# Kernel optimization log

Hardware: AMD Instinct MI355X
Metric: run time of the kernel (lower is better)

## Reference

```python
import jax, jax.numpy as jnp
import numpy as np

N, C, H, W = 4, 256, 32, 32
NH = 2                      # att_nhead
HD = C // NH                # 128 per-head dim
MAX_DIS = 7
WS = 2 * MAX_DIS + 1        # 15 window side
WW = WS * WS                # 225 window positions
T = (C / NH) ** 0.5


def _gather_idx(h, w):
    # idx[wpos, m]: flat index into zero-padded (h+14, w+14) grid of the
    # neighbor at window offset wpos for query pixel m (== F.unfold semantics)
    pw = w + 2 * MAX_DIS
    dy, dx = np.meshgrid(np.arange(WS), np.arange(WS), indexing='ij')
    ys, xs = np.meshgrid(np.arange(h), np.arange(w), indexing='ij')
    idx = (dy.reshape(-1, 1) + ys.reshape(1, -1)) * pw + (dx.reshape(-1, 1) + xs.reshape(1, -1))
    return jnp.asarray(idx, dtype=jnp.int32)  # [WW, h*w]


def setup_inputs() -> dict:
    key = jax.random.key(0)
    ks = jax.random.split(key, 14)
    s = 0.02
    return {
        'q': jax.random.normal(ks[0], (N, C, H, W), jnp.float32),
        'k': jax.random.normal(ks[1], (N, C, H, W), jnp.float32),
        'v': jax.random.normal(ks[2], (N, C, H, W), jnp.float32),
        'Wq': jax.random.normal(ks[3], (C, C), jnp.float32) * s,
        'bq': jnp.zeros((C,), jnp.float32),
        'Wk': jax.random.normal(ks[4], (C, C), jnp.float32) * s,
        'bk': jnp.zeros((C,), jnp.float32),
        'Wv': jax.random.normal(ks[5], (C, C), jnp.float32) * s,
        'bv': jnp.zeros((C,), jnp.float32),
        'Wrel': jax.random.normal(ks[6], (NH, WW, HD), jnp.float32) * s,   # grouped 1x1 conv
        'brel': jnp.zeros((NH * WW,), jnp.float32),
        'V_bias': jax.random.normal(ks[7], (NH, HD, WW), jnp.float32) * s,
        'Wfc': jax.random.normal(ks[8], (C, C), jnp.float32) * s,
        'bfc': jnp.zeros((C,), jnp.float32),
    }


def _conv1x1(x, Wt, b):
    return jnp.einsum('nchw,dc->ndhw', x, Wt) + b[None, :, None, None]


def reference(q, k, v, Wq, bq, Wk, bk, Wv, bv, Wrel, brel, V_bias, Wfc, bfc):
    n, c, h, w = q.shape
    hw = h * w
    idx = _gather_idx(h, w)                                   # [WW, hw]
    pad = ((0, 0), (0, 0), (0, 0), (MAX_DIS, MAX_DIS), (MAX_DIS, MAX_DIS))

    q = _conv1x1(q, Wq, bq)
    k = _conv1x1(k, Wk, bk)
    v = _conv1x1(v, Wv, bv)

    # grouped 1x1 conv: relative position logits, [n, NH, WW, hw]
    rel = jnp.einsum('ngcxy,gwc->ngwxy', q.reshape(n, NH, HD, h, w), Wrel)
    rel = rel + brel.reshape(NH, WW)[None, :, :, None, None]
    rel = rel.reshape(n, NH, WW, hw)

    qs = (q / T).reshape(n, NH, HD, hw)

    # unfold K via zero-pad + gather: [n, NH, HD, WW, hw]
    k_pad = jnp.pad(k.reshape(n, NH, HD, h, w), pad).reshape(n, NH, HD, -1)
    k_un = k_pad[..., idx]
    qk = jnp.einsum('ngcm,ngcwm->ngwm', qs, k_un) + rel

    # boundary mask: neighbor inside the original image
    valid = jnp.pad(jnp.ones((h, w), jnp.float32), MAX_DIS).reshape(-1)[idx] > 0
    qk = jnp.where(valid[None, None], qk, jnp.float32(-1e8))
    attn = jax.nn.softmax(qk, axis=2)                         # over window positions

    agg_bias = jnp.einsum('ngwm,gcw->mngc', attn, V_bias).reshape(hw, n, c)

    # local2global scatter + dense einsum == gather of zero-padded V
    v_pad = jnp.pad(v.reshape(n, NH, HD, h, w), pad).reshape(n, NH, HD, -1)
    v_un = v_pad[..., idx]                                    # [n, NH, HD, WW, hw]
    agg_value = jnp.einsum('ngwm,ngcwm->mngc', attn, v_un).reshape(hw, n, c)

    out = (agg_value + agg_bias) @ Wfc.T + bfc                # [hw, n, c]
    return out
```

## Files before the change

kernel.cpp:

```cpp
#include <hip/hip_runtime.h>
#include <math.h>


typedef __attribute__((ext_vector_type(8))) short short8;
typedef __attribute__((ext_vector_type(4))) short short4v;
typedef __attribute__((ext_vector_type(4))) float floatx4;

__device__ __forceinline__ short f2bf(float f) {
    unsigned u = __float_as_uint(f);
    unsigned r = (u + 0x7fffu + ((u >> 16) & 1u)) >> 16;
    return (short)r;
}
__device__ __forceinline__ float bf2f(short s) {
    return __uint_as_float(((unsigned)(unsigned short)s) << 16);
}

__global__ __launch_bounds__(256)
void conv_kernel(const float* __restrict__ q, const float* __restrict__ k,
                 const float* __restrict__ v,
                 const float* __restrict__ Wq, const float* __restrict__ Wk,
                 const float* __restrict__ Wv, const float* __restrict__ Wfc,
                 const float* __restrict__ Wrel,
                 short* __restrict__ Xhi, short* __restrict__ Xlo,
                 short* __restrict__ Whi, short* __restrict__ Wlo,
                 short* __restrict__ Wrh, short* __restrict__ Wrl)
{
    const int tid = threadIdx.x;
    const int z = blockIdx.z;
    const int lane = tid & 63;
    const int n16 = lane & 15, quad = lane >> 4;

    if (z < 12) {
        __shared__ float st[64 * 33];
        const int sel = z >> 2, batch = z & 3;
        const float* X = (sel == 0 ? q : sel == 1 ? k : v) + ((long)batch << 18);
        const int mb = blockIdx.x, kc = blockIdx.y;
#pragma unroll
        for (int it = 0; it < 8; ++it) {
            int e = tid + it * 256;
            int cc = e >> 6, mm = e & 63;
            st[mm * 33 + cc] = X[((long)(kc * 32 + cc) << 10) + mb * 64 + mm];
        }
        __syncthreads();
        const int mtl = tid >> 6;
        const int m = mtl * 16 + n16;
        short h[8], l[8];
#pragma unroll
        for (int j = 0; j < 8; ++j) {
            float f = st[m * 33 + quad * 8 + j];
            short hb = f2bf(f);
            h[j] = hb;
            l[j] = f2bf(f - bf2f(hb));
        }
        int mt16 = mb * 4 + mtl;
        long off = (long)z * 262144 + (((long)(mt16 * 8 + kc) * 64) + lane) * 8;
        *(short8*)(Xhi + off) = *(short8*)&h[0];
        *(short8*)(Xlo + off) = *(short8*)&l[0];
    } else if (z < 16) {
        if (tid >= 64) return;
        const int w = z - 12;
        const float* W = (w == 0 ? Wq : w == 1 ? Wk : w == 2 ? Wv : Wfc);
        const int dt = blockIdx.x, kc = blockIdx.y;
        const int d = dt * 16 + n16, cb = kc * 32 + quad * 8;
        float4 w0 = *(const float4*)&W[d * 256 + cb];
        float4 w1 = *(const float4*)&W[d * 256 + cb + 4];
        float f[8] = {w0.x, w0.y, w0.z, w0.w, w1.x, w1.y, w1.z, w1.w};
        short h[8], l[8];
#pragma unroll
        for (int j = 0; j < 8; ++j) {
            short hb = f2bf(f[j]);
            h[j] = hb;
            l[j] = f2bf(f[j] - bf2f(hb));
        }
        long off = (long)w * 65536 + (((long)(dt * 8 + kc) * 64) + lane) * 8;
        *(short8*)(Whi + off) = *(short8*)&h[0];
        *(short8*)(Wlo + off) = *(short8*)&l[0];
    } else {
        if (tid >= 64) return;
        const int g = z - 16;
        const int wt = blockIdx.x, kc = blockIdx.y;
        if (wt >= 15 || kc >= 4) return;
        const int w = wt * 16 + n16;
        const int cb = kc * 32 + quad * 8;
        float f[8] = {0.f, 0.f, 0.f, 0.f, 0.f, 0.f, 0.f, 0.f};
        if (w < 225) {
            float4 w0 = *(const float4*)&Wrel[(long)(g * 225 + w) * 128 + cb];
            float4 w1 = *(const float4*)&Wrel[(long)(g * 225 + w) * 128 + cb + 4];
            f[0] = w0.x; f[1] = w0.y; f[2] = w0.z; f[3] = w0.w;
            f[4] = w1.x; f[5] = w1.y; f[6] = w1.z; f[7] = w1.w;
        }
        short h[8], l[8];
#pragma unroll
        for (int j = 0; j < 8; ++j) {
            short hb = f2bf(f[j]);
            h[j] = hb;
            l[j] = f2bf(f[j] - bf2f(hb));
        }
        long off = (long)g * 30720 + (((long)(wt * 4 + kc) * 64) + lane) * 8;
        *(short8*)(Wrh + off) = *(short8*)&h[0];
        *(short8*)(Wrl + off) = *(short8*)&l[0];
    }
}

__global__ __launch_bounds__(256)
void mfma_proj(const short* __restrict__ Xhi, const short* __restrict__ Xlo,
               const short* __restrict__ Whi, const short* __restrict__ Wlo,
               const float* __restrict__ bq, const float* __restrict__ bk,
               const float* __restrict__ bv,
               short* __restrict__ qhi, short* __restrict__ qlo,
               short* __restrict__ khi, short* __restrict__ klo,
               float* __restrict__ vpad)
{
    __shared__ float tile[16 * 65];
    const int tid = threadIdx.x;
    const int wave = tid >> 6, lane = tid & 63;
    const int n16 = lane & 15, quad = lane >> 4;
    const int mt16 = blockIdx.x, db = blockIdx.y, z = blockIdx.z;
    const int sel = z >> 2, batch = z & 3;
    const int dt = db * 4 + wave;

    const short* Ah = Whi + (long)sel * 65536 + ((long)(dt * 8) * 64 + lane) * 8;
    const short* Al = Wlo + (long)sel * 65536 + ((long)(dt * 8) * 64 + lane) * 8;
    const short* Bh = Xhi + (long)z * 262144;
    const short* Bl = Xlo + (long)z * 262144;

    const float* bias = (sel == 0 ? bq : sel == 1 ? bk : bv);
    float4 bv4 = *(const float4*)&bias[dt * 16 + quad * 4];
    float bb[4] = {bv4.x, bv4.y, bv4.z, bv4.w};

    floatx4 acc = {0.f, 0.f, 0.f, 0.f};
#pragma unroll
    for (int kc = 0; kc < 8; ++kc) {
        short8 ahi = *(const short8*)(Ah + kc * 512);
        short8 alo = *(const short8*)(Al + kc * 512);
        long bo = ((long)(mt16 * 8 + kc) * 64 + lane) * 8;
        short8 bh = *(const short8*)(Bh + bo);
        short8 bl = *(const short8*)(Bl + bo);
        acc = __builtin_amdgcn_mfma_f32_16x16x32_bf16(ahi, bh, acc, 0, 0, 0);
        acc = __builtin_amdgcn_mfma_f32_16x16x32_bf16(ahi, bl, acc, 0, 0, 0);
        acc = __builtin_amdgcn_mfma_f32_16x16x32_bf16(alo, bh, acc, 0, 0, 0);
    }

    if (sel == 2) {
        const int m = mt16 * 16 + n16;
        float* Y = vpad + (long)batch * 393216;
        const int row = m >> 5, col = (m & 31) + 8;
#pragma unroll
        for (int r = 0; r < 4; ++r)
            Y[(long)(dt * 16 + quad * 4 + r) * 1536 + row * 48 + col] = acc[r] + bb[r];
        {
            const int prow = mt16 >> 1, side = mt16 & 1;
            const int ch_l = tid >> 2, f2 = (tid & 3) * 2;
            long po = (long)(db * 64 + ch_l) * 1536 + prow * 48 + side * 40 + f2;
            Y[po] = 0.f;
            Y[po + 1] = 0.f;
        }
        return;
    }

    const int cl = wave * 16 + quad * 4;
#pragma unroll
    for (int r = 0; r < 4; ++r)
        tile[n16 * 65 + cl + r] = acc[r] + bb[r];
    __syncthreads();

    const float scale = (sel == 1) ? 0.08838834764831845f : 1.0f;
    const int m_l = tid >> 4, c16 = (tid & 15) * 4;
    const int m = mt16 * 16 + m_l;
    const int cglob = db * 64 + c16;
    const int g = cglob >> 7, ch = cglob & 127;
    const long base = (((long)(batch * 2 + g) << 10) + m) * 128 + ch;
    short h[4], l[4];
#pragma unroll
    for (int j = 0; j < 4; ++j) {
        float f = tile[m_l * 65 + c16 + j] * scale;
        short hb = f2bf(f);
        h[j] = hb;
        l[j] = f2bf(f - bf2f(hb));
    }
    short* oh = sel ? khi : qhi;
    short* ol = sel ? klo : qlo;
    *(short4v*)(oh + base) = *(short4v*)&h[0];
    *(short4v*)(ol + base) = *(short4v*)&l[0];
}

__global__ __launch_bounds__(256)
void scores_pv(const short* __restrict__ qhi, const short* __restrict__ qlo,
               const short* __restrict__ khi, const short* __restrict__ klo,
               const short* __restrict__ Wrh, const short* __restrict__ Wrl,
               const float* __restrict__ brel,
               const float* __restrict__ vpad, const float* __restrict__ Vbias,
               short* __restrict__ AGhi, short* __restrict__ AGlo)
{
    __shared__ __align__(16) float smem[16 * 241 + 225 * 16];
    __shared__ float invl[16];
    float* qk   = smem;
    float* pa2  = smem + 16 * 241;
    float* tile = smem;

    const int tid = threadIdx.x;
    const int wave = tid >> 6, lane = tid & 63;
    const int lin = blockIdx.x;
    const int bz  = lin & 7;
    const int r2  = lin >> 3;
    const int chh = r2 & 1;
    const int yy  = r2 >> 1;
    const int y   = yy >> 1;
    const int xt  = yy & 1;
    const int g = bz & 1;
    const int x0 = xt * 16;

    const int n16 = lane & 15, quad = lane >> 4;
    const long qbase = (((long)bz << 10) + y * 32 + x0 + n16) * 128 + quad * 8;
    short8 a_hi[4], a_lo[4];
#pragma unroll
    for (int ch = 0; ch < 4; ++ch) {
        a_hi[ch] = *(const short8*)(qhi + qbase + ch * 32);
        a_lo[ch] = *(const short8*)(qlo + qbase + ch * 32);
    }

    for (int wt = wave; wt < 15; wt += 4) {
        const short* Ah = Wrh + (long)g * 30720 + ((long)(wt * 4) * 64 + lane) * 8;
        const short* Al = Wrl + (long)g * 30720 + ((long)(wt * 4) * 64 + lane) * 8;
        floatx4 racc = {0.f, 0.f, 0.f, 0.f};
#pragma unroll
        for (int kc = 0; kc < 4; ++kc) {
            short8 whh = *(const short8*)(Ah + kc * 512);
            short8 wll = *(const short8*)(Al + kc * 512);
            racc = __builtin_amdgcn_mfma_f32_16x16x32_bf16(whh, a_hi[kc], racc, 0, 0, 0);
            racc = __builtin_amdgcn_mfma_f32_16x16x32_bf16(whh, a_lo[kc], racc, 0, 0, 0);
            racc = __builtin_amdgcn_mfma_f32_16x16x32_bf16(wll, a_hi[kc], racc, 0, 0, 0);
        }
#pragma unroll
        for (int r = 0; r < 4; ++r) {
            int w = wt * 16 + quad * 4 + r;
            if (w < 225) {
                int dy = w / 15, dx = w - dy * 15;
                qk[n16 * 241 + dy * 16 + dx] = racc[r] + brel[g * 225 + w];
            }
        }
    }
    __syncthreads();

    for (int e = tid; e < 16 * 241; e += 256) {
        int px = e / 241, idx = e - px * 241;
        int dy = idx >> 4, dx = idx & 15;
        int hy = y + dy - 7, hx = x0 + px + dx - 7;
        bool valid = (dx < 15) && (dy < 15) &&
                     (hy >= 0) && (hy < 32) && (hx >= 0) && (hx < 32);
        if (!valid) qk[e] = -1e8f;
    }
    __syncthreads();

    for (int dy = wave; dy < 15; dy += 4) {
        const int ky = y + dy - 7;
        if (ky < 0 || ky > 31) continue;
#pragma unroll
        for (int kxt = 0; kxt < 2; ++kxt) {
            const int kxg = x0 - 8 + kxt * 16 + n16;
            const long kb = (((long)bz << 10) + ky * 32 + kxg) * 128 + quad * 8;
            floatx4 acc = {0.f, 0.f, 0.f, 0.f};
#pragma unroll
            for (int ch = 0; ch < 4; ++ch) {
                short8 b_hi = *(const short8*)(khi + kb + ch * 32);
                short8 b_lo = *(const short8*)(klo + kb + ch * 32);
                acc = __builtin_amdgcn_mfma_f32_16x16x32_bf16(a_hi[ch], b_hi, acc, 0, 0, 0);
                acc = __builtin_amdgcn_mfma_f32_16x16x32_bf16(a_hi[ch], b_lo, acc, 0, 0, 0);
                acc = __builtin_amdgcn_mfma_f32_16x16x32_bf16(a_lo[ch], b_hi, acc, 0, 0, 0);
            }
            if (kxg >= 0 && kxg < 32) {
#pragma unroll
                for (int r = 0; r < 4; ++r) {
                    int m = quad * 4 + r;
                    int dx = kxg - (x0 + m) + 7;
                    if (dx >= 0 && dx < 15) {
                        int s = m * 241 + dy * 16 + dx;
                        qk[s] = qk[s] + acc[r];
                    }
                }
            }
        }
    }
    __syncthreads();

    {
        int px = tid >> 4, s = tid & 15;
        float mx = -3.0e38f;
        for (int w = s; w < 240; w += 16) mx = fmaxf(mx, qk[px * 241 + w]);
#pragma unroll
        for (int msk = 8; msk; msk >>= 1) mx = fmaxf(mx, __shfl_xor(mx, msk));
        float sum = 0.f;
        for (int w = s; w < 240; w += 16) {
            float p = __expf(qk[px * 241 + w] - mx);
            qk[px * 241 + w] = p;
            sum += p;
        }
#pragma unroll
        for (int msk = 8; msk; msk >>= 1) sum += __shfl_xor(sum, msk);
        if (s == 0) invl[px] = 1.0f / sum;
    }
    __syncthreads();

    for (int e = tid; e < 3600; e += 256) {
        int w = e >> 4, px = e & 15;
        int dy2 = w / 15, dx2 = w - dy2 * 15;
        pa2[w * 16 + px] = qk[px * 241 + dy2 * 16 + dx2] * invl[px];
    }
    __syncthreads();

    const int n = bz >> 1;
    const int chg = tid >> 2;
    const int xq  = tid & 3;
    const int c0  = chh * 64 + chg;
    const int xb  = x0 + xq * 4;
    const float* v0 = vpad + (long)bz * 196608 + (long)c0 * 1536;
    const float* b0 = Vbias + (g * 128 + c0) * 225;

    float acc0[4] = {0.f, 0.f, 0.f, 0.f};

    for (int dy = 0; dy < 15; ++dy) {
        int hy = y + dy - 7;
        if (hy < 0 || hy > 31) continue;
        const float4* r0 = (const float4*)(v0 + hy * 48 + xb);
        float wa[20];
#pragma unroll
        for (int t = 0; t < 5; ++t) {
            float4 a = r0[t];
            wa[4*t+0] = a.x; wa[4*t+1] = a.y; wa[4*t+2] = a.z; wa[4*t+3] = a.w;
        }
        const float* par = &pa2[dy * 15 * 16 + xq * 4];
        const float* vb0 = b0 + dy * 15;
#pragma unroll
        for (int dx = 0; dx < 15; ++dx) {
            float4 p4 = *(const float4*)&par[dx * 16];
            float ba = vb0[dx];
            acc0[0] += p4.x * (wa[1 + dx] + ba);
            acc0[1] += p4.y * (wa[2 + dx] + ba);
            acc0[2] += p4.z * (wa[3 + dx] + ba);
            acc0[3] += p4.w * (wa[4 + dx] + ba);
        }
    }

#pragma unroll
    for (int i = 0; i < 4; ++i)
        tile[(xq * 4 + i) * 68 + chg] = acc0[i];
    __syncthreads();

    const int sub = tid >> 6;
    if (sub < 2) {
        short h[8], l[8];
#pragma unroll
        for (int j = 0; j < 8; ++j) {
            float f = tile[n16 * 68 + sub * 32 + quad * 8 + j];
            short hb = f2bf(f);
            h[j] = hb;
            l[j] = f2bf(f - bf2f(hb));
        }
        const int mt16 = y * 2 + xt;
        const int kc = g * 4 + chh * 2 + sub;
        long off = (long)n * 262144 + (((long)(mt16 * 8 + kc) * 64) + lane) * 8;
        *(short8*)(AGhi + off) = *(short8*)&h[0];
        *(short8*)(AGlo + off) = *(short8*)&l[0];
    }
}

__global__ __launch_bounds__(256)
void mfma_fc(const short* __restrict__ Ahi, const short* __restrict__ Alo,
             const short* __restrict__ Whi, const short* __restrict__ Wlo,
             const float* __restrict__ bfc, float* __restrict__ out)
{
    __shared__ float tile[16 * 68];
    const int tid = threadIdx.x;
    const int wave = tid >> 6, lane = tid & 63;
    const int n16 = lane & 15, quad = lane >> 4;
    const int mt16 = blockIdx.x, db = blockIdx.y, nz = blockIdx.z;
    const int dt = db * 4 + wave;

    const short* Ah = Whi + (long)3 * 65536 + ((long)(dt * 8) * 64 + lane) * 8;
    const short* Al = Wlo + (long)3 * 65536 + ((long)(dt * 8) * 64 + lane) * 8;
    const short* Bh = Ahi + (long)nz * 262144;
    const short* Bl = Alo + (long)nz * 262144;

    float4 bv4 = *(const float4*)&bfc[dt * 16 + quad * 4];
    float bb[4] = {bv4.x, bv4.y, bv4.z, bv4.w};

    floatx4 acc = {0.f, 0.f, 0.f, 0.f};
#pragma unroll
    for (int kc = 0; kc < 8; ++kc) {
        short8 ahi = *(const short8*)(Ah + kc * 512);
        short8 alo = *(const short8*)(Al + kc * 512);
        long bo = ((long)(mt16 * 8 + kc) * 64 + lane) * 8;
        short8 bh = *(const short8*)(Bh + bo);
        short8 bl = *(const short8*)(Bl + bo);
        acc = __builtin_amdgcn_mfma_f32_16x16x32_bf16(ahi, bh, acc, 0, 0, 0);
        acc = __builtin_amdgcn_mfma_f32_16x16x32_bf16(ahi, bl, acc, 0, 0, 0);
        acc = __builtin_amdgcn_mfma_f32_16x16x32_bf16(alo, bh, acc, 0, 0, 0);
    }

    const int dl = wave * 16 + quad * 4;
#pragma unroll
    for (int r = 0; r < 4; ++r)
        tile[n16 * 68 + dl + r] = acc[r] + bb[r];
    __syncthreads();

    const int mm = tid >> 4, d4 = (tid & 15) * 4;
    float4 o4 = *(const float4*)&tile[mm * 68 + d4];
    *(float4*)&out[(long)(mt16 * 16 + mm) * 1024 + nz * 256 + db * 64 + d4] = o4;
}

extern "C" void kernel_launch(void* const* d_in, const int* in_sizes, int n_in,
                              void* d_out, int out_size, void* d_ws, size_t ws_size,
                              hipStream_t stream)
{
    const float* q    = (const float*)d_in[0];
    const float* k    = (const float*)d_in[1];
    const float* v    = (const float*)d_in[2];
    const float* Wq   = (const float*)d_in[3];
    const float* bq   = (const float*)d_in[4];
    const float* Wk   = (const float*)d_in[5];
    const float* bk   = (const float*)d_in[6];
    const float* Wv   = (const float*)d_in[7];
    const float* bv   = (const float*)d_in[8];
    const float* Wrel = (const float*)d_in[9];
    const float* brel = (const float*)d_in[10];
    const float* Vb   = (const float*)d_in[11];
    const float* Wfc  = (const float*)d_in[12];
    const float* bfc  = (const float*)d_in[13];
    float* out = (float*)d_out;

    float* ws   = (float*)d_ws;
    float* vpad = ws + 2097152;
    short* qhi  = (short*)(ws + 6561792);
    short* qlo  = (short*)(ws + 7086080);
    short* khi  = (short*)(ws + 7610368);
    short* klo  = (short*)(ws + 8134656);
    short* Xhi  = (short*)(ws + 8658944);
    short* Xlo  = (short*)(ws + 10231808);
    short* Whi  = (short*)(ws + 11804672);
    short* Wlo  = (short*)(ws + 11935744);
    short* AGhi = (short*)(ws + 12066816);
    short* AGlo = (short*)(ws + 12591104);
    short* Wrh  = (short*)(ws + 13115392);
    short* Wrl  = (short*)(ws + 13146112);

    dim3 blk(256);

    conv_kernel<<<dim3(16, 8, 18), blk, 0, stream>>>(q, k, v, Wq, Wk, Wv, Wfc,
                                                     Wrel, Xhi, Xlo, Whi, Wlo,
                                                     Wrh, Wrl);

    mfma_proj<<<dim3(64, 4, 12), blk, 0, stream>>>(Xhi, Xlo, Whi, Wlo,
                                                   bq, bk, bv,
                                                   qhi, qlo, khi, klo, vpad);

    scores_pv<<<dim3(1024), blk, 0, stream>>>(qhi, qlo, khi, klo,
                                              Wrh, Wrl, brel,
                                              vpad, Vb, AGhi, AGlo);

    mfma_fc<<<dim3(64, 4, 4), blk, 0, stream>>>(AGhi, AGlo, Whi, Wlo, bfc, out);
}
```

Baseline: 167.5 us.

## Fuse activation bf16 split into projection GEMM and widen per-block output tiles

The separate pass that converted q/k/v activations into hi/lo bf16 tiles in workspace is removed. The projection kernel now loads raw fp32 activations into shared memory and does the split on the fly, with each block covering all 256 output channels for a 16-pixel tile. This saves a full write and read of the intermediate X buffers and one kernel's worth of work. The FC kernel also computes two output tiles per wave to reuse B fragments, and several conversions now use native short8 vectors. The cost is fewer, larger blocks: 768 instead of 3072 projection blocks, which lowers parallelism and raises register and shared-memory pressure.

```diff
diff --git a/kernel.cpp b/kernel.cpp
--- a/kernel.cpp
+++ b/kernel.cpp
@@ -15,69 +15,36 @@
     return __uint_as_float(((unsigned)(unsigned short)s) << 16);
 }
 
-__global__ __launch_bounds__(256)
-void conv_kernel(const float* __restrict__ q, const float* __restrict__ k,
-                 const float* __restrict__ v,
-                 const float* __restrict__ Wq, const float* __restrict__ Wk,
-                 const float* __restrict__ Wv, const float* __restrict__ Wfc,
-                 const float* __restrict__ Wrel,
-                 short* __restrict__ Xhi, short* __restrict__ Xlo,
-                 short* __restrict__ Whi, short* __restrict__ Wlo,
-                 short* __restrict__ Wrh, short* __restrict__ Wrl)
+__global__ __launch_bounds__(64)
+void conv_w(const float* __restrict__ Wq, const float* __restrict__ Wk,
+            const float* __restrict__ Wv, const float* __restrict__ Wfc,
+            const float* __restrict__ Wrel,
+            short* __restrict__ Whi, short* __restrict__ Wlo,
+            short* __restrict__ Wrh, short* __restrict__ Wrl)
 {
-    const int tid = threadIdx.x;
+    const int lane = threadIdx.x;
+    const int n16 = lane & 15, quad = lane >> 4;
     const int z = blockIdx.z;
-    const int lane = tid & 63;
-    const int n16 = lane & 15, quad = lane >> 4;
-
-    if (z < 12) {
-        __shared__ float st[64 * 33];
-        const int sel = z >> 2, batch = z & 3;
-        const float* X = (sel == 0 ? q : sel == 1 ? k : v) + ((long)batch << 18);
-        const int mb = blockIdx.x, kc = blockIdx.y;
-#pragma unroll
-        for (int it = 0; it < 8; ++it) {
-            int e = tid + it * 256;
-            int cc = e >> 6, mm = e & 63;
-            st[mm * 33 + cc] = X[((long)(kc * 32 + cc) << 10) + mb * 64 + mm];
-        }
-        __syncthreads();
-        const int mtl = tid >> 6;
-        const int m = mtl * 16 + n16;
-        short h[8], l[8];
-#pragma unroll
-        for (int j = 0; j < 8; ++j) {
-            float f = st[m * 33 + quad * 8 + j];
-            short hb = f2bf(f);
-            h[j] = hb;
-            l[j] = f2bf(f - bf2f(hb));
-        }
-        int mt16 = mb * 4 + mtl;
-        long off = (long)z * 262144 + (((long)(mt16 * 8 + kc) * 64) + lane) * 8;
-        *(short8*)(Xhi + off) = *(short8*)&h[0];
-        *(short8*)(Xlo + off) = *(short8*)&l[0];
-    } else if (z < 16) {
-        if (tid >= 64) return;
-        const int w = z - 12;
-        const float* W = (w == 0 ? Wq : w == 1 ? Wk : w == 2 ? Wv : Wfc);
+
+    if (z < 4) {
+        const float* W = (z == 0 ? Wq : z == 1 ? Wk : z == 2 ? Wv : Wfc);
         const int dt = blockIdx.x, kc = blockIdx.y;
         const int d = dt * 16 + n16, cb = kc * 32 + quad * 8;
         float4 w0 = *(const float4*)&W[d * 256 + cb];
         float4 w1 = *(const float4*)&W[d * 256 + cb + 4];
         float f[8] = {w0.x, w0.y, w0.z, w0.w, w1.x, w1.y, w1.z, w1.w};
-        short h[8], l[8];
+        short8 h8, l8;
 #pragma unroll
         for (int j = 0; j < 8; ++j) {
             short hb = f2bf(f[j]);
-            h[j] = hb;
-            l[j] = f2bf(f[j] - bf2f(hb));
-        }
-        long off = (long)w * 65536 + (((long)(dt * 8 + kc) * 64) + lane) * 8;
-        *(short8*)(Whi + off) = *(short8*)&h[0];
-        *(short8*)(Wlo + off) = *(short8*)&l[0];
+            h8[j] = hb;
+            l8[j] = f2bf(f[j] - bf2f(hb));
+        }
+        long off = (long)z * 65536 + (((long)(dt * 8 + kc) * 64) + lane) * 8;
+        *(short8*)(Whi + off) = h8;
+        *(short8*)(Wlo + off) = l8;
     } else {
-        if (tid >= 64) return;
-        const int g = z - 16;
+        const int g = z - 4;
         const int wt = blockIdx.x, kc = blockIdx.y;
         if (wt >= 15 || kc >= 4) return;
         const int w = wt * 16 + n16;
@@ -89,21 +56,22 @@
             f[0] = w0.x; f[1] = w0.y; f[2] = w0.z; f[3] = w0.w;
             f[4] = w1.x; f[5] = w1.y; f[6] = w1.z; f[7] = w1.w;
         }
-        short h[8], l[8];
+        short8 h8, l8;
 #pragma unroll
         for (int j = 0; j < 8; ++j) {
             short hb = f2bf(f[j]);
-            h[j] = hb;
-            l[j] = f2bf(f[j] - bf2f(hb));
+            h8[j] = hb;
+            l8[j] = f2bf(f[j] - bf2f(hb));
         }
         long off = (long)g * 30720 + (((long)(wt * 4 + kc) * 64) + lane) * 8;
-        *(short8*)(Wrh + off) = *(short8*)&h[0];
-        *(short8*)(Wrl + off) = *(short8*)&l[0];
+        *(short8*)(Wrh + off) = h8;
+        *(short8*)(Wrl + off) = l8;
     }
 }
 
 __global__ __launch_bounds__(256)
-void mfma_proj(const short* __restrict__ Xhi, const short* __restrict__ Xlo,
+void mfma_proj(const float* __restrict__ q, const float* __restrict__ k,
+               const float* __restrict__ v,
                const short* __restrict__ Whi, const short* __restrict__ Wlo,
                const float* __restrict__ bq, const float* __restrict__ bk,
                const float* __restrict__ bv,
@@ -111,77 +79,115 @@
                short* __restrict__ khi, short* __restrict__ klo,
                float* __restrict__ vpad)
 {
-    __shared__ float tile[16 * 65];
+    __shared__ float st[256 * 17];
     const int tid = threadIdx.x;
     const int wave = tid >> 6, lane = tid & 63;
     const int n16 = lane & 15, quad = lane >> 4;
-    const int mt16 = blockIdx.x, db = blockIdx.y, z = blockIdx.z;
+    const int mt16 = blockIdx.x, z = blockIdx.y;
     const int sel = z >> 2, batch = z & 3;
-    const int dt = db * 4 + wave;
-
-    const short* Ah = Whi + (long)sel * 65536 + ((long)(dt * 8) * 64 + lane) * 8;
-    const short* Al = Wlo + (long)sel * 65536 + ((long)(dt * 8) * 64 + lane) * 8;
-    const short* Bh = Xhi + (long)z * 262144;
-    const short* Bl = Xlo + (long)z * 262144;
+
+    const float* X = (sel == 0 ? q : sel == 1 ? k : v) + ((long)batch << 18);
+
+    {
+        const float* src = X + ((long)tid << 10) + mt16 * 16;
+        float4 a0 = *(const float4*)(src);
+        float4 a1 = *(const float4*)(src + 4);
+        float4 a2 = *(const float4*)(src + 8);
+        float4 a3 = *(const float4*)(src + 12);
+        float* d = &st[tid * 17];
+        d[0] = a0.x; d[1] = a0.y; d[2] = a0.z; d[3] = a0.w;
+        d[4] = a1.x; d[5] = a1.y; d[6] = a1.z; d[7] = a1.w;
+        d[8] = a2.x; d[9] = a2.y; d[10] = a2.z; d[11] = a2.w;
+        d[12] = a3.x; d[13] = a3.y; d[14] = a3.z; d[15] = a3.w;
+    }
 
     const float* bias = (sel == 0 ? bq : sel == 1 ? bk : bv);
-    float4 bv4 = *(const float4*)&bias[dt * 16 + quad * 4];
-    float bb[4] = {bv4.x, bv4.y, bv4.z, bv4.w};
-
-    floatx4 acc = {0.f, 0.f, 0.f, 0.f};
+    float bbv[4][4];
+#pragma unroll
+    for (int i = 0; i < 4; ++i) {
+        float4 b4 = *(const float4*)&bias[(wave * 4 + i) * 16 + quad * 4];
+        bbv[i][0] = b4.x; bbv[i][1] = b4.y; bbv[i][2] = b4.z; bbv[i][3] = b4.w;
+    }
+    __syncthreads();
+
+    floatx4 acc[4] = {{0.f,0.f,0.f,0.f},{0.f,0.f,0.f,0.f},
+                      {0.f,0.f,0.f,0.f},{0.f,0.f,0.f,0.f}};
+    const long abase = (long)sel * 65536 + (long)lane * 8;
 #pragma unroll
     for (int kc = 0; kc < 8; ++kc) {
-        short8 ahi = *(const short8*)(Ah + kc * 512);
-        short8 alo = *(const short8*)(Al + kc * 512);
-        long bo = ((long)(mt16 * 8 + kc) * 64 + lane) * 8;
-        short8 bh = *(const short8*)(Bh + bo);
-        short8 bl = *(const short8*)(Bl + bo);
-        acc = __builtin_amdgcn_mfma_f32_16x16x32_bf16(ahi, bh, acc, 0, 0, 0);
-        acc = __builtin_amdgcn_mfma_f32_16x16x32_bf16(ahi, bl, acc, 0, 0, 0);
-        acc = __builtin_amdgcn_mfma_f32_16x16x32_bf16(alo, bh, acc, 0, 0, 0);
+        short8 bh, bl;
+        const float* col = &st[(kc * 32 + quad * 8) * 17 + n16];
+#pragma unroll
+        for (int j = 0; j < 8; ++j) {
+            float f = col[j * 17];
+            short hb = f2bf(f);
+            bh[j] = hb;
+            bl[j] = f2bf(f - bf2f(hb));
+        }
+#pragma unroll
+        for (int i = 0; i < 4; ++i) {
+            const int dt = wave * 4 + i;
+            short8 ahi = *(const short8*)(Whi + abase + (long)(dt * 8 + kc) * 512);
+            short8 alo = *(const short8*)(Wlo + abase + (long)(dt * 8 + kc) * 512);
+            acc[i] = __builtin_amdgcn_mfma_f32_16x16x32_bf16(ahi, bh, acc[i], 0, 0, 0);
+            acc[i] = __builtin_amdgcn_mfma_f32_16x16x32_bf16(ahi, bl, acc[i], 0, 0, 0);
+            acc[i] = __builtin_amdgcn_mfma_f32_16x16x32_bf16(alo, bh, acc[i], 0, 0, 0);
+        }
     }
 
     if (sel == 2) {
+        float* Y = vpad + (long)batch * 393216;
         const int m = mt16 * 16 + n16;
-        float* Y = vpad + (long)batch * 393216;
         const int row = m >> 5, col = (m & 31) + 8;
 #pragma unroll
-        for (int r = 0; r < 4; ++r)
-            Y[(long)(dt * 16 + quad * 4 + r) * 1536 + row * 48 + col] = acc[r] + bb[r];
+        for (int i = 0; i < 4; ++i) {
+            const int dt = wave * 4 + i;
+#pragma unroll
+            for (int r = 0; r < 4; ++r)
+                Y[(long)(dt * 16 + quad * 4 + r) * 1536 + row * 48 + col] = acc[i][r] + bbv[i][r];
+        }
         {
             const int prow = mt16 >> 1, side = mt16 & 1;
-            const int ch_l = tid >> 2, f2 = (tid & 3) * 2;
-            long po = (long)(db * 64 + ch_l) * 1536 + prow * 48 + side * 40 + f2;
-            Y[po] = 0.f;
-            Y[po + 1] = 0.f;
+            long po = (long)tid * 1536 + prow * 48 + side * 40;
+            float4 zz = {0.f, 0.f, 0.f, 0.f};
+            *(float4*)&Y[po] = zz;
+            *(float4*)&Y[po + 4] = zz;
         }
         return;
     }
 
-    const int cl = wave * 16 + quad * 4;
-#pragma unroll
-    for (int r = 0; r < 4; ++r)
-        tile[n16 * 65 + cl + r] = acc[r] + bb[r];
+    __syncthreads();
+    float* tile = st;
+#pragma unroll
+    for (int i = 0; i < 4; ++i) {
+        const int dt = wave * 4 + i;
+#pragma unroll
+        for (int r = 0; r < 4; ++r)
+            tile[n16 * 257 + dt * 16 + quad * 4 + r] = acc[i][r] + bbv[i][r];
+    }
     __syncthreads();
 
     const float scale = (sel == 1) ? 0.08838834764831845f : 1.0f;
-    const int m_l = tid >> 4, c16 = (tid & 15) * 4;
+    const int m_l = tid >> 4, c16 = (tid & 15) * 16;
     const int m = mt16 * 16 + m_l;
-    const int cglob = db * 64 + c16;
-    const int g = cglob >> 7, ch = cglob & 127;
-    const long base = (((long)(batch * 2 + g) << 10) + m) * 128 + ch;
-    short h[4], l[4];
-#pragma unroll
-    for (int j = 0; j < 4; ++j) {
-        float f = tile[m_l * 65 + c16 + j] * scale;
-        short hb = f2bf(f);
-        h[j] = hb;
-        l[j] = f2bf(f - bf2f(hb));
-    }
     short* oh = sel ? khi : qhi;
     short* ol = sel ? klo : qlo;
-    *(short4v*)(oh + base) = *(short4v*)&h[0];
-    *(short4v*)(ol + base) = *(short4v*)&l[0];
+#pragma unroll
+    for (int half = 0; half < 2; ++half) {
+        const int cg = c16 + half * 8;
+        short8 h8, l8;
+#pragma unroll
+        for (int j = 0; j < 8; ++j) {
+            float f = tile[m_l * 257 + cg + j] * scale;
+            short hb = f2bf(f);
+            h8[j] = hb;
+            l8[j] = f2bf(f - bf2f(hb));
+        }
+        const int g = cg >> 7, ch = cg & 127;
+        const long base = (((long)(batch * 2 + g) << 10) + m) * 128 + ch;
+        *(short8*)(oh + base) = h8;
+        *(short8*)(ol + base) = l8;
+    }
 }
 
 __global__ __launch_bounds__(256)
@@ -348,19 +354,19 @@
 
     const int sub = tid >> 6;
     if (sub < 2) {
-        short h[8], l[8];
+        short8 h8, l8;
 #pragma unroll
         for (int j = 0; j < 8; ++j) {
             float f = tile[n16 * 68 + sub * 32 + quad * 8 + j];
             short hb = f2bf(f);
-            h[j] = hb;
-            l[j] = f2bf(f - bf2f(hb));
+            h8[j] = hb;
+            l8[j] = f2bf(f - bf2f(hb));
         }
         const int mt16 = y * 2 + xt;
         const int kc = g * 4 + chh * 2 + sub;
         long off = (long)n * 262144 + (((long)(mt16 * 8 + kc) * 64) + lane) * 8;
-        *(short8*)(AGhi + off) = *(short8*)&h[0];
-        *(short8*)(AGlo + off) = *(short8*)&l[0];
+        *(short8*)(AGhi + off) = h8;
+        *(short8*)(AGlo + off) = l8;
     }
 }
 
@@ -369,43 +375,56 @@
              const short* __restrict__ Whi, const short* __restrict__ Wlo,
              const float* __restrict__ bfc, float* __restrict__ out)
 {
-    __shared__ float tile[16 * 68];
+    __shared__ float tile[16 * 132];
     const int tid = threadIdx.x;
     const int wave = tid >> 6, lane = tid & 63;
     const int n16 = lane & 15, quad = lane >> 4;
-    const int mt16 = blockIdx.x, db = blockIdx.y, nz = blockIdx.z;
-    const int dt = db * 4 + wave;
-
-    const short* Ah = Whi + (long)3 * 65536 + ((long)(dt * 8) * 64 + lane) * 8;
-    const short* Al = Wlo + (long)3 * 65536 + ((long)(dt * 8) * 64 + lane) * 8;
+    const int mt16 = blockIdx.x, db2 = blockIdx.y, nz = blockIdx.z;
+    const int dt0 = db2 * 8 + wave * 2;
+
     const short* Bh = Ahi + (long)nz * 262144;
     const short* Bl = Alo + (long)nz * 262144;
-
-    float4 bv4 = *(const float4*)&bfc[dt * 16 + quad * 4];
-    float bb[4] = {bv4.x, bv4.y, bv4.z, bv4.w};
-
-    floatx4 acc = {0.f, 0.f, 0.f, 0.f};
+    const long abase = (long)3 * 65536 + (long)lane * 8;
+
+    float bbv[2][4];
+#pragma unroll
+    for (int p = 0; p < 2; ++p) {
+        float4 b4 = *(const float4*)&bfc[(dt0 + p) * 16 + quad * 4];
+        bbv[p][0] = b4.x; bbv[p][1] = b4.y; bbv[p][2] = b4.z; bbv[p][3] = b4.w;
+    }
+
+    floatx4 acc[2] = {{0.f,0.f,0.f,0.f},{0.f,0.f,0.f,0.f}};
 #pragma unroll
     for (int kc = 0; kc < 8; ++kc) {
-        short8 ahi = *(const short8*)(Ah + kc * 512);
-        short8 alo = *(const short8*)(Al + kc * 512);
-        long bo = ((long)(mt16 * 8 + kc) * 64 + lane) * 8;
+        const long bo = (long)(mt16 * 8 + kc) * 512 + (long)lane * 8;
         short8 bh = *(const short8*)(Bh + bo);
         short8 bl = *(const short8*)(Bl + bo);
-        acc = __builtin_amdgcn_mfma_f32_16x16x32_bf16(ahi, bh, acc, 0, 0, 0);
-        acc = __builtin_amdgcn_mfma_f32_16x16x32_bf16(ahi, bl, acc, 0, 0, 0);
-        acc = __builtin_amdgcn_mfma_f32_16x16x32_bf16(alo, bh, acc, 0, 0, 0);
-    }
-
-    const int dl = wave * 16 + quad * 4;
-#pragma unroll
-    for (int r = 0; r < 4; ++r)
-        tile[n16 * 68 + dl + r] = acc[r] + bb[r];
-    __syncthreads();
-
-    const int mm = tid >> 4, d4 = (tid & 15) * 4;
-    float4 o4 = *(const float4*)&tile[mm * 68 + d4];
-    *(float4*)&out[(long)(mt16 * 16 + mm) * 1024 + nz * 256 + db * 64 + d4] = o4;
+#pragma unroll
+        for (int p = 0; p < 2; ++p) {
+            const int dt = dt0 + p;
+            short8 ahi = *(const short8*)(Whi + abase + (long)(dt * 8 + kc) * 512);
+            short8 alo = *(const short8*)(Wlo + abase + (long)(dt * 8 + kc) * 512);
+            acc[p] = __builtin_amdgcn_mfma_f32_16x16x32_bf16(ahi, bh, acc[p], 0, 0, 0);
+            acc[p] = __builtin_amdgcn_mfma_f32_16x16x32_bf16(ahi, bl, acc[p], 0, 0, 0);
+            acc[p] = __builtin_amdgcn_mfma_f32_16x16x32_bf16(alo, bh, acc[p], 0, 0, 0);
+        }
+    }
+
+#pragma unroll
+    for (int p = 0; p < 2; ++p) {
+        const int dl = (wave * 2 + p) * 16 + quad * 4;
+#pragma unroll
+        for (int r = 0; r < 4; ++r)
+            tile[n16 * 132 + dl + r] = acc[p][r] + bbv[p][r];
+    }
+    __syncthreads();
+
+    const int m_l = tid >> 4, d8 = (tid & 15) * 8;
+    float4 o0 = *(const float4*)&tile[m_l * 132 + d8];
+    float4 o1 = *(const float4*)&tile[m_l * 132 + d8 + 4];
+    long ob = (long)(mt16 * 16 + m_l) * 1024 + nz * 256 + db2 * 128 + d8;
+    *(float4*)&out[ob] = o0;
+    *(float4*)&out[ob + 4] = o1;
 }
 
 extern "C" void kernel_launch(void* const* d_in, const int* in_sizes, int n_in,
@@ -434,8 +453,6 @@
     short* qlo  = (short*)(ws + 7086080);
     short* khi  = (short*)(ws + 7610368);
     short* klo  = (short*)(ws + 8134656);
-    short* Xhi  = (short*)(ws + 8658944);
-    short* Xlo  = (short*)(ws + 10231808);
     short* Whi  = (short*)(ws + 11804672);
     short* Wlo  = (short*)(ws + 11935744);
     short* AGhi = (short*)(ws + 12066816);
@@ -443,19 +460,17 @@
     short* Wrh  = (short*)(ws + 13115392);
     short* Wrl  = (short*)(ws + 13146112);
 
-    dim3 blk(256);
-
-    conv_kernel<<<dim3(16, 8, 18), blk, 0, stream>>>(q, k, v, Wq, Wk, Wv, Wfc,
-                                                     Wrel, Xhi, Xlo, Whi, Wlo,
-                                                     Wrh, Wrl);
-
-    mfma_proj<<<dim3(64, 4, 12), blk, 0, stream>>>(Xhi, Xlo, Whi, Wlo,
-                                                   bq, bk, bv,
-                                                   qhi, qlo, khi, klo, vpad);
-
-    scores_pv<<<dim3(1024), blk, 0, stream>>>(qhi, qlo, khi, klo,
-                                              Wrh, Wrl, brel,
-                                              vpad, Vb, AGhi, AGlo);
-
-    mfma_fc<<<dim3(64, 4, 4), blk, 0, stream>>>(AGhi, AGlo, Whi, Wlo, bfc, out);
-}
+    conv_w<<<dim3(16, 8, 6), dim3(64), 0, stream>>>(Wq, Wk, Wv, Wfc, Wrel,
+                                                    Whi, Wlo, Wrh, Wrl);
+
+    mfma_proj<<<dim3(64, 12), dim3(256), 0, stream>>>(q, k, v, Whi, Wlo,
+                                                      bq, bk, bv,
+                                                      qhi, qlo, khi, klo, vpad);
+
+    scores_pv<<<dim3(1024), dim3(256), 0, stream>>>(qhi, qlo, khi, klo,
+                                                    Wrh, Wrl, brel,
+                                                    vpad, Vb, AGhi, AGlo);
+
+    mfma_fc<<<dim3(64, 2, 4), dim3(256), 0, stream>>>(AGhi, AGlo, Whi, Wlo,
+                                                      bfc, out);
+}
```

After: 171.5 us. 1.02x slower.
